# Kernel optimization log

Measured on AMD Instinct MI355X. Metric: run time of the kernel, lower is better.

The kernel has to match this reference:

```python
import jax, jax.numpy as jnp
import numpy as np

N = 50000   # nodes
E = 800000  # edges
F = 128     # num_node_features
H = 256     # hidden_channels
C = 40      # num_classes


def setup_inputs() -> dict:
    key = jax.random.key(0)
    ks = jax.random.split(key, 8)
    x = jax.random.normal(ks[0], (N, F), dtype=jnp.float32)
    edge_index = jax.random.randint(ks[1], (2, E), 0, N, dtype=jnp.int32)
    # GCNConv linear weights (PyG: lin has no bias; bias added post-aggregation)
    W1 = jax.random.normal(ks[2], (H, F), dtype=jnp.float32) * (1.0 / np.sqrt(F))
    b1 = jnp.zeros((H,), dtype=jnp.float32)
    W2 = jax.random.normal(ks[3], (H, H), dtype=jnp.float32) * (1.0 / np.sqrt(H))
    b2 = jnp.zeros((H,), dtype=jnp.float32)
    Wout = jax.random.normal(ks[4], (C, H), dtype=jnp.float32) * (1.0 / np.sqrt(H))
    bout = jnp.zeros((C,), dtype=jnp.float32)
    return {"x": x, "edge_index": edge_index,
            "W1": W1, "b1": b1, "W2": W2, "b2": b2,
            "Wout": Wout, "bout": bout}


def gcn_conv(x, src, dst, W, b, n):
    """PyG GCNConv: sym-normalized aggregation with self-loops.
    deg computed as in-degree on dst (gcn_norm), +1 for self loop.
    """
    h = x @ W.T  # [n, out]
    ones = jnp.ones((src.shape[0],), dtype=h.dtype)
    deg = jax.ops.segment_sum(ones, dst, num_segments=n) + 1.0  # self loop
    dinv = jax.lax.rsqrt(deg)  # deg >= 1, safe
    norm = dinv[src] * dinv[dst]                 # [E]
    agg = jax.ops.segment_sum(norm[:, None] * h[src], dst, num_segments=n)
    agg = agg + (dinv * dinv)[:, None] * h       # self-loop term
    return agg + b


def reference(x, edge_index, W1, b1, W2, b2, Wout, bout):
    src, dst = edge_index[0], edge_index[1]
    h = jax.nn.relu(gcn_conv(x, src, dst, W1, b1, N))
    h = gcn_conv(h, src, dst, W2, b2, N)
    return h @ Wout.T + bout  # [N, C] logits
```

## Files before the change

kernel.cpp:

```cpp
#include <hip/hip_runtime.h>

#define N_NODES 50000
#define N_EDGES 800000
#define F_IN    128
#define H_DIM   256
#define C_OUT   40
#define MT_TOT  (N_NODES / 16)
#define NBIN1   196
#define NCHB    200
#define CHSZ    (N_EDGES / NCHB)
#define CVT_X   (N_NODES * F_IN / 4)
#define CVT_W1B (H_DIM * F_IN / 4 / 256)

typedef unsigned short u16;
typedef unsigned int   u32;
typedef short bf16x8 __attribute__((ext_vector_type(8)));
typedef float f32x4  __attribute__((ext_vector_type(4)));

__device__ inline float bfbits2f(u16 u) { return __uint_as_float(((u32)u) << 16); }
__device__ inline u16 f2bf(float f) {
    u32 u = __float_as_uint(f);
    u += 0x7fffu + ((u >> 16) & 1u);
    return (u16)(u >> 16);
}
__device__ inline u32 pack2(float a, float b) {
    return (u32)f2bf(a) | ((u32)f2bf(b) << 16);
}

__global__ __launch_bounds__(256) void pre_k(const int* __restrict__ dst, int* __restrict__ Ht,
                                             const float4* __restrict__ W1, uint2* __restrict__ W1b,
                                             const float* __restrict__ W2, const float* __restrict__ Wo,
                                             const float* __restrict__ b2, const float* __restrict__ bo,
                                             u16* __restrict__ Wcb, float* __restrict__ bc,
                                             int* __restrict__ done) {
    __shared__ int hist[NBIN1];
    __shared__ float red[256];
    const int t = threadIdx.x;
    if (blockIdx.x < NCHB) {
        const int b = blockIdx.x;
        if (b == 0 && t == 0) *done = 0;
        if (t < NBIN1) hist[t] = 0;
        __syncthreads();
        for (int i = b * CHSZ + t; i < (b + 1) * CHSZ; i += 256)
            atomicAdd(&hist[dst[i] >> 8], 1);
        __syncthreads();
        if (t < NBIN1) Ht[t * NCHB + b] = hist[t];
        return;
    }
    if (blockIdx.x < NCHB + CVT_W1B) {
        int i = (blockIdx.x - NCHB) * 256 + t;
        float4 v = W1[i];
        uint2 o; o.x = pack2(v.x, v.y); o.y = pack2(v.z, v.w);
        W1b[i] = o;
        return;
    }
    const int c = blockIdx.x - NCHB - CVT_W1B;
    float acc = 0.f;
    for (int o = 0; o < H_DIM; o += 8) {
        float w2v[8];
#pragma unroll
        for (int j = 0; j < 8; j++) w2v[j] = W2[(size_t)(o + j) * H_DIM + t];
#pragma unroll
        for (int j = 0; j < 8; j++) acc += Wo[(size_t)c * H_DIM + o + j] * w2v[j];
    }
    Wcb[(size_t)c * H_DIM + t] = f2bf(acc);
    red[t] = b2[t] * Wo[(size_t)c * H_DIM + t];
    __syncthreads();
    for (int off = 128; off > 0; off >>= 1) {
        if (t < off) red[t] += red[t + off];
        __syncthreads();
    }
    if (t == 0) bc[c] = red[0] + bo[c];
}

__global__ __launch_bounds__(256) void scan_k(int* __restrict__ Ht, int* __restrict__ totals,
                                              int* __restrict__ base, int* __restrict__ rowptr,
                                              int* __restrict__ done) {
    __shared__ int sc[256];
    __shared__ int lastflag;
    const int t = threadIdx.x;
    const int g = blockIdx.x;
    int v = (t < NCHB) ? Ht[g * NCHB + t] : 0;
    sc[t] = v;
    __syncthreads();
    for (int off = 1; off < 256; off <<= 1) {
        int u = (t >= off) ? sc[t - off] : 0;
        __syncthreads();
        sc[t] += u;
        __syncthreads();
    }
    if (t < NCHB) Ht[g * NCHB + t] = sc[t] - v;
    if (t == NCHB - 1)
        __hip_atomic_store(&totals[g], sc[t], __ATOMIC_RELAXED, __HIP_MEMORY_SCOPE_AGENT);
    __syncthreads();
    if (t == 0) {
        int old = __hip_atomic_fetch_add(done, 1, __ATOMIC_ACQ_REL, __HIP_MEMORY_SCOPE_AGENT);
        lastflag = (old == NBIN1 - 1);
    }
    __syncthreads();
    if (!lastflag) return;
    int tv = (t < NBIN1) ? __hip_atomic_load(&totals[t], __ATOMIC_RELAXED, __HIP_MEMORY_SCOPE_AGENT) : 0;
    sc[t] = tv;
    __syncthreads();
    for (int off = 1; off < 256; off <<= 1) {
        int u = (t >= off) ? sc[t - off] : 0;
        __syncthreads();
        sc[t] += u;
        __syncthreads();
    }
    if (t < NBIN1) base[t] = sc[t] - tv;
    if (t == NBIN1 - 1) base[NBIN1] = sc[t];
    if (t == 0) rowptr[N_NODES] = N_EDGES;
}

__global__ __launch_bounds__(256) void p2scatter_k(const int* __restrict__ src, const int* __restrict__ dst,
                                                   const int* __restrict__ Ht, const int* __restrict__ base,
                                                   uint2* __restrict__ T) {
    __shared__ int cur[NBIN1];
    const int t = threadIdx.x;
    const int b = blockIdx.x;
    if (t < NBIN1) cur[t] = base[t] + Ht[t * NCHB + b];
    __syncthreads();
    for (int i = b * CHSZ + t; i < (b + 1) * CHSZ; i += 256) {
        const int s = src[i], d = dst[i];
        const int pos = atomicAdd(&cur[d >> 8], 1);
        uint2 ed; ed.x = (u32)s; ed.y = (u32)d;
        T[pos] = ed;
    }
}

__global__ __launch_bounds__(256) void p3x_k(const uint2* __restrict__ T, const int* __restrict__ base,
                                             int* __restrict__ rowptr, float* __restrict__ dinv,
                                             u32* __restrict__ edata,
                                             const float4* __restrict__ x, uint2* __restrict__ xb) {
    __shared__ int hcnt[256];
    __shared__ int sc[256];
    __shared__ int cur[256];
    __shared__ float sdinv[256];
    const int t = threadIdx.x;
    const int g = blockIdx.x;
    const int nbeg = base[g], nend = base[g + 1];
    hcnt[t] = 0;
    __syncthreads();
    for (int i = nbeg + t; i < nend; i += 256)
        atomicAdd(&hcnt[T[i].y & 255], 1);
    __syncthreads();
    const int my = hcnt[t];
    sc[t] = my;
    __syncthreads();
    for (int off = 1; off < 256; off <<= 1) {
        int u = (t >= off) ? sc[t - off] : 0;
        __syncthreads();
        sc[t] += u;
        __syncthreads();
    }
    const int rbeg = nbeg + sc[t] - my;
    const int node = g * 256 + t;
    const float dv = rsqrtf((float)my + 1.0f);
    sdinv[t] = dv;
    if (node < N_NODES) {
        rowptr[node] = rbeg;
        dinv[node] = dv;
    }
    cur[t] = rbeg;
    __syncthreads();
    for (int i = nbeg + t; i < nend; i += 256) {
        const uint2 e = T[i];
        const int pos = atomicAdd(&cur[e.y & 255], 1);
        edata[pos] = e.x;
    }
    const int gbase = g * 256 * (F_IN / 4);
    for (int i = t; i < 256 * (F_IN / 4); i += 256) {
        const int gi = gbase + i;
        if (gi >= CVT_X) break;
        const float s = sdinv[i >> 5];
        float4 v = x[gi];
        uint2 o; o.x = pack2(s * v.x, s * v.y); o.y = pack2(s * v.z, s * v.w);
        xb[gi] = o;
    }
}

__global__ __launch_bounds__(256) void gather1_k(const u32* __restrict__ xb,
                                                 const int* __restrict__ rowptr,
                                                 const u32* __restrict__ edata,
                                                 const float* __restrict__ dinv,
                                                 u32* __restrict__ aggx) {
    const int node = __builtin_amdgcn_readfirstlane(blockIdx.x * 4 + (threadIdx.x >> 6));
    const int lane = threadIdx.x & 63;
    if (node >= N_NODES) return;
    const int beg = __builtin_amdgcn_readfirstlane(rowptr[node]);
    const int end = __builtin_amdgcn_readfirstlane(rowptr[node + 1]);
    const float dd = dinv[node];
    const u32 vs = xb[(size_t)node * 64 + lane];
    float a0 = bfbits2f((u16)vs);
    float a1 = bfbits2f((u16)(vs >> 16));
    int e = beg;
    for (; e + 7 < end; e += 8) {
        u32 s8[8];
#pragma unroll
        for (int j = 0; j < 8; j++) s8[j] = edata[e + j];
        u32 v[8];
#pragma unroll
        for (int j = 0; j < 8; j++) v[j] = xb[(size_t)s8[j] * 64 + lane];
#pragma unroll
        for (int j = 0; j < 8; j++) {
            a0 += bfbits2f((u16)v[j]);
            a1 += bfbits2f((u16)(v[j] >> 16));
        }
    }
    for (; e < end; e++) {
        const u32 v0 = xb[(size_t)edata[e] * 64 + lane];
        a0 += bfbits2f((u16)v0);
        a1 += bfbits2f((u16)(v0 >> 16));
    }
    aggx[(size_t)node * 64 + lane] = pack2(dd * a0, dd * a1);
}

__global__ __launch_bounds__(256) void bgemm1f_k(const u16* __restrict__ X,
                                                 const u16* __restrict__ W1b,
                                                 const float* __restrict__ b1,
                                                 const u16* __restrict__ Wcb,
                                                 const float* __restrict__ dinv,
                                                 u16* __restrict__ tb) {
    constexpr int KF1 = F_IN / 32;
    constexpr int KF2 = H_DIM / 32;
    __shared__ __align__(16) u16 hs[2][16][H_DIM + 8];
    const int wave = threadIdx.x >> 6;
    const int lane = threadIdx.x & 63;
    const int quad = lane >> 4;
    const int nn = lane & 15;
    const int ngbase = wave * 64;

    bf16x8 Bf[4][KF1];
    float bb[4];
#pragma unroll
    for (int j = 0; j < 4; j++) {
        const int wr = ngbase + j * 16 + nn;
#pragma unroll
        for (int kf = 0; kf < KF1; kf++)
            Bf[j][kf] = *(const bf16x8*)(W1b + (size_t)wr * F_IN + kf * 32 + quad * 8);
        bb[j] = b1[wr];
    }
    bf16x8 Bh[KF2];
    {
        int hr = wave * 16 + nn;
        if (hr > C_OUT - 1) hr = C_OUT - 1;
#pragma unroll
        for (int kf = 0; kf < KF2; kf++)
            Bh[kf] = *(const bf16x8*)(Wcb + (size_t)hr * H_DIM + kf * 32 + quad * 8);
    }

    int mt = blockIdx.x;
    if (mt >= MT_TOT) return;
    const int stride = gridDim.x;
    int buf = 0;

    bf16x8 Acur[KF1], Anext[KF1];
    {
        const u16* ap = X + (size_t)(mt * 16 + nn) * F_IN + quad * 8;
#pragma unroll
        for (int kf = 0; kf < KF1; kf++) Acur[kf] = *(const bf16x8*)(ap + kf * 32);
    }

    while (true) {
        const int mtn = mt + stride;
        if (mtn < MT_TOT) {
            const u16* ap = X + (size_t)(mtn * 16 + nn) * F_IN + quad * 8;
#pragma unroll
            for (int kf = 0; kf < KF1; kf++) Anext[kf] = *(const bf16x8*)(ap + kf * 32);
        }

        f32x4 acc[4];
#pragma unroll
        for (int j = 0; j < 4; j++) acc[j] = (f32x4){0.f, 0.f, 0.f, 0.f};
#pragma unroll
        for (int kf = 0; kf < KF1; kf++)
#pragma unroll
            for (int j = 0; j < 4; j++)
                acc[j] = __builtin_amdgcn_mfma_f32_16x16x32_bf16(Acur[kf], Bf[j][kf], acc[j], 0, 0, 0);

#pragma unroll
        for (int j = 0; j < 4; j++)
#pragma unroll
            for (int r = 0; r < 4; r++)
                hs[buf][quad * 4 + r][ngbase + j * 16 + nn] = f2bf(fmaxf(acc[j][r] + bb[j], 0.f));
        __syncthreads();

        if (wave < 3) {
            f32x4 ah = (f32x4){0.f, 0.f, 0.f, 0.f};
#pragma unroll
            for (int kf = 0; kf < KF2; kf++) {
                bf16x8 af = *(const bf16x8*)(&hs[buf][nn][kf * 32 + quad * 8]);
                ah = __builtin_amdgcn_mfma_f32_16x16x32_bf16(af, Bh[kf], ah, 0, 0, 0);
            }
            const int col = wave * 16 + nn;
            if (col < C_OUT) {
#pragma unroll
                for (int r = 0; r < 4; r++) {
                    const int row = mt * 16 + quad * 4 + r;
                    tb[(size_t)row * C_OUT + col] = f2bf(dinv[row] * ah[r]);
                }
            }
        }

        if (mtn >= MT_TOT) break;
#pragma unroll
        for (int kf = 0; kf < KF1; kf++) Acur[kf] = Anext[kf];
        mt = mtn;
        buf ^= 1;
    }
}

__global__ __launch_bounds__(256) void gatherO_k(const u32* __restrict__ tb,
                                                 const int* __restrict__ rowptr,
                                                 const u32* __restrict__ edata,
                                                 const float* __restrict__ dinv,
                                                 const float* __restrict__ bc,
                                                 float* __restrict__ out) {
    const int node = __builtin_amdgcn_readfirstlane(blockIdx.x * 4 + (threadIdx.x >> 6));
    const int lane = threadIdx.x & 63;
    if (node >= N_NODES) return;
    const int lc = lane & 31;
    const bool act = (lc < C_OUT / 2);
    const int beg = __builtin_amdgcn_readfirstlane(rowptr[node]);
    const int end = __builtin_amdgcn_readfirstlane(rowptr[node + 1]);
    const float dd = dinv[node];
    const u32 vs = act ? tb[(size_t)node * (C_OUT / 2) + lc] : 0u;
    float a0 = bfbits2f((u16)vs);
    float a1 = bfbits2f((u16)(vs >> 16));
    int e = beg;
    for (; e + 7 < end; e += 8) {
        u32 s8[8];
#pragma unroll
        for (int j = 0; j < 8; j++) s8[j] = edata[e + j];
        u32 v[8];
#pragma unroll
        for (int j = 0; j < 8; j++) v[j] = act ? tb[(size_t)s8[j] * (C_OUT / 2) + lc] : 0u;
#pragma unroll
        for (int j = 0; j < 8; j++) {
            a0 += bfbits2f((u16)v[j]);
            a1 += bfbits2f((u16)(v[j] >> 16));
        }
    }
    for (; e < end; e++) {
        const u32 v0 = act ? tb[(size_t)edata[e] * (C_OUT / 2) + lc] : 0u;
        a0 += bfbits2f((u16)v0);
        a1 += bfbits2f((u16)(v0 >> 16));
    }
    if (lane < C_OUT / 2) {
        float2 o;
        o.x = dd * a0 + bc[2 * lane];
        o.y = dd * a1 + bc[2 * lane + 1];
        *(float2*)(out + (size_t)node * C_OUT + 2 * lane) = o;
    }
}

extern "C" void kernel_launch(void* const* d_in, const int* in_sizes, int n_in,
                              void* d_out, int out_size, void* d_ws, size_t ws_size,
                              hipStream_t stream) {
    const float* x    = (const float*)d_in[0];
    const int*   ei   = (const int*)d_in[1];
    const float* W1   = (const float*)d_in[2];
    const float* b1   = (const float*)d_in[3];
    const float* W2   = (const float*)d_in[4];
    const float* b2   = (const float*)d_in[5];
    const float* Wout = (const float*)d_in[6];
    const float* bout = (const float*)d_in[7];
    float* out = (float*)d_out;

    const int* src = ei;
    const int* dst = ei + N_EDGES;

    char* ws = (char*)d_ws;
    size_t o = 0;
    auto alloc = [&](size_t bytes) { size_t p = o; o = (o + bytes + 255) & ~(size_t)255; return p; };
    int*   Ht     = (int*)(ws + alloc((size_t)NBIN1 * NCHB * 4));
    int*   totals = (int*)(ws + alloc((size_t)NBIN1 * 4));
    int*   base   = (int*)(ws + alloc((size_t)(NBIN1 + 1) * 4));
    float* dinv   = (float*)(ws + alloc((size_t)N_NODES * 4));
    int*   rowptr = (int*)(ws + alloc((size_t)(N_NODES + 1) * 4));
    uint2* T      = (uint2*)(ws + alloc((size_t)N_EDGES * 8));
    u32*   edata  = (u32*)(ws + alloc((size_t)N_EDGES * 4));
    u16*   xb     = (u16*)(ws + alloc((size_t)N_NODES * F_IN * 2));
    u16*   aggxb  = (u16*)(ws + alloc((size_t)N_NODES * F_IN * 2));
    u16*   tb     = (u16*)(ws + alloc((size_t)N_NODES * C_OUT * 2 + 256));
    u16*   W1b    = (u16*)(ws + alloc((size_t)H_DIM * F_IN * 2));
    u16*   Wcb    = (u16*)(ws + alloc((size_t)C_OUT * H_DIM * 2));
    float* bc     = (float*)(ws + alloc((size_t)C_OUT * 4));
    int*   done   = (int*)(ws + alloc(256));

    pre_k<<<NCHB + CVT_W1B + C_OUT, 256, 0, stream>>>(
        dst, Ht, (const float4*)W1, (uint2*)W1b, W2, Wout, b2, bout, Wcb, bc, done);
    scan_k<<<NBIN1, 256, 0, stream>>>(Ht, totals, base, rowptr, done);
    p2scatter_k<<<NCHB, 256, 0, stream>>>(src, dst, Ht, base, T);
    p3x_k<<<NBIN1, 256, 0, stream>>>(T, base, rowptr, dinv, edata, (const float4*)x, (uint2*)xb);

    gather1_k<<<(N_NODES + 3) / 4, 256, 0, stream>>>((const u32*)xb, rowptr, edata, dinv, (u32*)aggxb);
    bgemm1f_k<<<768, 256, 0, stream>>>(aggxb, W1b, b1, Wcb, dinv, tb);
    gatherO_k<<<(N_NODES + 3) / 4, 256, 0, stream>>>((const u32*)tb, rowptr, edata, dinv, bc, out);
}
```

Baseline: 196.8 us.

## Fuse first-layer neighbor gather into the persistent GEMM kernel via LDS staging

The standalone gather kernel is removed. Each 16-node tile's neighbor aggregation is now done inside the persistent bf16 MFMA GEMM kernel and staged through a double-buffered, XOR-swizzled LDS tile. This eliminates the aggregated-feature intermediate buffer, its global write and read, and one kernel launch. The gather for the next tile is issued between the MFMA stage and the barrier to overlap it with the output projection. The trade-off is that the latency-bound gather now runs with far fewer waves in flight (a 768-block grid), which could reduce memory-latency hiding.

```diff
diff --git a/kernel.cpp b/kernel.cpp
--- a/kernel.cpp
+++ b/kernel.cpp
@@ -180,51 +180,18 @@
     }
 }
 
-__global__ __launch_bounds__(256) void gather1_k(const u32* __restrict__ xb,
+__global__ __launch_bounds__(256) void bgemm1g_k(const u32* __restrict__ xb,
                                                  const int* __restrict__ rowptr,
                                                  const u32* __restrict__ edata,
                                                  const float* __restrict__ dinv,
-                                                 u32* __restrict__ aggx) {
-    const int node = __builtin_amdgcn_readfirstlane(blockIdx.x * 4 + (threadIdx.x >> 6));
-    const int lane = threadIdx.x & 63;
-    if (node >= N_NODES) return;
-    const int beg = __builtin_amdgcn_readfirstlane(rowptr[node]);
-    const int end = __builtin_amdgcn_readfirstlane(rowptr[node + 1]);
-    const float dd = dinv[node];
-    const u32 vs = xb[(size_t)node * 64 + lane];
-    float a0 = bfbits2f((u16)vs);
-    float a1 = bfbits2f((u16)(vs >> 16));
-    int e = beg;
-    for (; e + 7 < end; e += 8) {
-        u32 s8[8];
-#pragma unroll
-        for (int j = 0; j < 8; j++) s8[j] = edata[e + j];
-        u32 v[8];
-#pragma unroll
-        for (int j = 0; j < 8; j++) v[j] = xb[(size_t)s8[j] * 64 + lane];
-#pragma unroll
-        for (int j = 0; j < 8; j++) {
-            a0 += bfbits2f((u16)v[j]);
-            a1 += bfbits2f((u16)(v[j] >> 16));
-        }
-    }
-    for (; e < end; e++) {
-        const u32 v0 = xb[(size_t)edata[e] * 64 + lane];
-        a0 += bfbits2f((u16)v0);
-        a1 += bfbits2f((u16)(v0 >> 16));
-    }
-    aggx[(size_t)node * 64 + lane] = pack2(dd * a0, dd * a1);
-}
-
-__global__ __launch_bounds__(256) void bgemm1f_k(const u16* __restrict__ X,
                                                  const u16* __restrict__ W1b,
                                                  const float* __restrict__ b1,
                                                  const u16* __restrict__ Wcb,
-                                                 const float* __restrict__ dinv,
                                                  u16* __restrict__ tb) {
     constexpr int KF1 = F_IN / 32;
     constexpr int KF2 = H_DIM / 32;
     __shared__ __align__(16) u16 hs[2][16][H_DIM + 8];
+    __shared__ __align__(16) u32 As[2][16][64];
     const int wave = threadIdx.x >> 6;
     const int lane = threadIdx.x & 63;
     const int quad = lane >> 4;
@@ -255,20 +222,50 @@
     const int stride = gridDim.x;
     int buf = 0;
 
-    bf16x8 Acur[KF1], Anext[KF1];
-    {
-        const u16* ap = X + (size_t)(mt * 16 + nn) * F_IN + quad * 8;
-#pragma unroll
-        for (int kf = 0; kf < KF1; kf++) Acur[kf] = *(const bf16x8*)(ap + kf * 32);
-    }
+    auto gather_tile = [&](int mtx, int b) {
+#pragma unroll 1
+        for (int i = 0; i < 4; i++) {
+            const int node = mtx * 16 + wave * 4 + i;
+            const int beg = __builtin_amdgcn_readfirstlane(rowptr[node]);
+            const int end = __builtin_amdgcn_readfirstlane(rowptr[node + 1]);
+            const float dd = dinv[node];
+            const u32 vs = xb[(size_t)node * 64 + lane];
+            float a0 = bfbits2f((u16)vs);
+            float a1 = bfbits2f((u16)(vs >> 16));
+            int e = beg;
+            for (; e + 7 < end; e += 8) {
+                u32 s8[8];
+#pragma unroll
+                for (int j = 0; j < 8; j++) s8[j] = edata[e + j];
+                u32 v[8];
+#pragma unroll
+                for (int j = 0; j < 8; j++) v[j] = xb[(size_t)s8[j] * 64 + lane];
+#pragma unroll
+                for (int j = 0; j < 8; j++) {
+                    a0 += bfbits2f((u16)v[j]);
+                    a1 += bfbits2f((u16)(v[j] >> 16));
+                }
+            }
+            for (; e < end; e++) {
+                const u32 v0 = xb[(size_t)edata[e] * 64 + lane];
+                a0 += bfbits2f((u16)v0);
+                a1 += bfbits2f((u16)(v0 >> 16));
+            }
+            const int row = wave * 4 + i;
+            As[b][row][lane ^ ((row & 7) << 2)] = pack2(dd * a0, dd * a1);
+        }
+    };
+
+    gather_tile(mt, 0);
+    __syncthreads();
 
     while (true) {
         const int mtn = mt + stride;
-        if (mtn < MT_TOT) {
-            const u16* ap = X + (size_t)(mtn * 16 + nn) * F_IN + quad * 8;
-#pragma unroll
-            for (int kf = 0; kf < KF1; kf++) Anext[kf] = *(const bf16x8*)(ap + kf * 32);
-        }
+
+        bf16x8 Af[KF1];
+#pragma unroll
+        for (int kf = 0; kf < KF1; kf++)
+            Af[kf] = *(const bf16x8*)&As[buf][nn][(kf * 16 + quad * 4) ^ ((nn & 7) << 2)];
 
         f32x4 acc[4];
 #pragma unroll
@@ -277,13 +274,15 @@
         for (int kf = 0; kf < KF1; kf++)
 #pragma unroll
             for (int j = 0; j < 4; j++)
-                acc[j] = __builtin_amdgcn_mfma_f32_16x16x32_bf16(Acur[kf], Bf[j][kf], acc[j], 0, 0, 0);
+                acc[j] = __builtin_amdgcn_mfma_f32_16x16x32_bf16(Af[kf], Bf[j][kf], acc[j], 0, 0, 0);
 
 #pragma unroll
         for (int j = 0; j < 4; j++)
 #pragma unroll
             for (int r = 0; r < 4; r++)
                 hs[buf][quad * 4 + r][ngbase + j * 16 + nn] = f2bf(fmaxf(acc[j][r] + bb[j], 0.f));
+
+        if (mtn < MT_TOT) gather_tile(mtn, buf ^ 1);
         __syncthreads();
 
         if (wave < 3) {
@@ -304,8 +303,6 @@
         }
 
         if (mtn >= MT_TOT) break;
-#pragma unroll
-        for (int kf = 0; kf < KF1; kf++) Acur[kf] = Anext[kf];
         mt = mtn;
         buf ^= 1;
     }
@@ -382,7 +379,6 @@
     uint2* T      = (uint2*)(ws + alloc((size_t)N_EDGES * 8));
     u32*   edata  = (u32*)(ws + alloc((size_t)N_EDGES * 4));
     u16*   xb     = (u16*)(ws + alloc((size_t)N_NODES * F_IN * 2));
-    u16*   aggxb  = (u16*)(ws + alloc((size_t)N_NODES * F_IN * 2));
     u16*   tb     = (u16*)(ws + alloc((size_t)N_NODES * C_OUT * 2 + 256));
     u16*   W1b    = (u16*)(ws + alloc((size_t)H_DIM * F_IN * 2));
     u16*   Wcb    = (u16*)(ws + alloc((size_t)C_OUT * H_DIM * 2));
@@ -395,7 +391,6 @@
     p2scatter_k<<<NCHB, 256, 0, stream>>>(src, dst, Ht, base, T);
     p3x_k<<<NBIN1, 256, 0, stream>>>(T, base, rowptr, dinv, edata, (const float4*)x, (uint2*)xb);
 
-    gather1_k<<<(N_NODES + 3) / 4, 256, 0, stream>>>((const u32*)xb, rowptr, edata, dinv, (u32*)aggxb);
-    bgemm1f_k<<<768, 256, 0, stream>>>(aggxb, W1b, b1, Wcb, dinv, tb);
+    bgemm1g_k<<<768, 256, 0, stream>>>((const u32*)xb, rowptr, edata, dinv, W1b, b1, Wcb, tb);
     gatherO_k<<<(N_NODES + 3) / 4, 256, 0, stream>>>((const u32*)tb, rowptr, edata, dinv, bc, out);
 }
```

Result: slower. 221.2 us (+12.4%).
